# Kernel tuning notes

Hardware: AMD Instinct MI355X
Metric: run time of the kernel (lower is better)

## Reference

```python
import jax, jax.numpy as jnp
import numpy as np
from jax import lax

EPS = 1e-6

def build_hh_matrix(V):
    """V: [d, d] rows are (unnormalized) Householder vectors.
    Returns Q = prod_i (I - 2 v_i v_i^T) applied left-to-right, matching
    the torch loop Q <- Q @ (I - 2 v v^T) == Q - 2 (Q v) v^T (rank-1 update)."""
    d = V.shape[0]
    Vn = V / (jnp.linalg.norm(V, axis=1, keepdims=True) + EPS)
    def step(Q, v):
        Qv = Q @ v                      # [d]
        return Q - 2.0 * jnp.outer(Qv, v), None
    Q, _ = lax.scan(step, jnp.eye(d, dtype=V.dtype), Vn)
    return Q


def setup_inputs() -> dict:
    key = jax.random.key(0)
    k1, k2 = jax.random.split(key)
    x = jax.random.normal(k1, (131072, 512), dtype=jnp.float32)
    hd_vecs = jax.random.normal(k2, (1, 512, 512), dtype=jnp.float32)
    return {"x": x, "hd_vecs": hd_vecs}


def reference(x, hd_vecs):
    # n_mat == 1 branch: out = (Q @ x^T)^T = x @ Q^T
    Q = build_hh_matrix(hd_vecs[0])     # [d, d]
    return x @ Q.T                      # [npatches, d]
```

## Files before the change

kernel.cpp:

```cpp
#include <hip/hip_runtime.h>
#include <hip/hip_bf16.h>
#include <stdint.h>

#define EPS 1e-6f

typedef unsigned short ushort_t;
using frag  = __attribute__((ext_vector_type(8))) short;
using f32x4 = __attribute__((ext_vector_type(4))) float;
using fv4   = __attribute__((ext_vector_type(4))) float;

__device__ __forceinline__ ushort_t f2bf(float f) {
  uint32_t u = __builtin_bit_cast(uint32_t, f);
  u += 0x7FFFu + ((u >> 16) & 1u);
  return (ushort_t)(u >> 16);
}

__global__ __launch_bounds__(256) void normalize_kernel(const float* __restrict__ V,
                                                        float* __restrict__ Vn) {
  const int gw   = blockIdx.x * 4 + (threadIdx.x >> 6);
  const int lane = threadIdx.x & 63;
  const float4* src = (const float4*)(V + gw * 512) + lane * 2;
  float4 a = src[0], c = src[1];
  float s = a.x*a.x + a.y*a.y + a.z*a.z + a.w*a.w
          + c.x*c.x + c.y*c.y + c.z*c.z + c.w*c.w;
  #pragma unroll
  for (int off = 32; off; off >>= 1) s += __shfl_xor(s, off);
  float inv = 1.f / (sqrtf(s) + EPS);
  float4 na = make_float4(a.x*inv, a.y*inv, a.z*inv, a.w*inv);
  float4 nc = make_float4(c.x*inv, c.y*inv, c.z*inv, c.w*inv);
  float4* dst = (float4*)(Vn + gw * 512) + lane * 2;
  dst[0] = na; dst[1] = nc;
}

__global__ __launch_bounds__(256) void gram_kernel(const float* __restrict__ Vn,
                                                   float* __restrict__ G) {
  const int gw   = blockIdx.x * 4 + (threadIdx.x >> 6);
  const int b    = gw >> 7, i = gw & 127;
  const int lane = threadIdx.x & 63;
  const float4* ri = (const float4*)(Vn + (b * 128 + i) * 512) + lane * 2;
  float4 a0 = ri[0], a1 = ri[1];
  #pragma unroll 2
  for (int j = i + 1; j < 128; ++j) {
    const float4* rj = (const float4*)(Vn + (b * 128 + j) * 512) + lane * 2;
    float4 c0 = rj[0], c1 = rj[1];
    float s = a0.x*c0.x + a0.y*c0.y + a0.z*c0.z + a0.w*c0.w
            + a1.x*c1.x + a1.y*c1.y + a1.z*c1.z + a1.w*c1.w;
    #pragma unroll
    for (int off = 32; off; off >>= 1) s += __shfl_xor(s, off);
    if (lane == 0) G[(b * 128 + i) * 128 + j] = s;
  }
}

__global__ __launch_bounds__(256) void trinv_kernel(float* __restrict__ GT) {
  __shared__ float Gs[128][132];
  __shared__ float Ai[64][68];
  __shared__ float Di[64][68];
  __shared__ float C1[64][68];
  const int b = blockIdx.x, tid = threadIdx.x;
  float* Gg = GT + b * 16384;

  {
    const int r = tid >> 1, h = tid & 1;
    const float4* src = (const float4*)(Gg + r * 128 + h * 64);
    float4* dst = (float4*)(&Gs[r][h * 64]);
    #pragma unroll
    for (int e = 0; e < 16; ++e) dst[e] = src[e];
  }
  __syncthreads();

  const int wave = tid >> 6, lane = tid & 63;
  if (wave < 2) {
    const int o = wave * 64;
    float t[64];
    #pragma unroll
    for (int i = 63; i >= 0; --i) {
      float s = (i == lane) ? 1.f : 0.f;
      #pragma unroll
      for (int j = i + 1; j < 64; ++j) s -= Gs[o + i][o + j] * t[j];
      t[i] = 2.f * s;
    }
    float (*OUT)[68] = wave ? Di : Ai;
    #pragma unroll
    for (int i = 0; i < 64; ++i) OUT[i][lane] = t[i];
  }
  __syncthreads();

  const int i0 = (tid >> 4) << 2;
  const int j0 = (tid & 15) << 2;

  {
    fv4 acc[4] = {};
    for (int l = 0; l < 64; l += 4) {
      fv4 g[4], d[4];
      #pragma unroll
      for (int r = 0; r < 4; ++r) g[r] = *(const fv4*)(&Gs[i0 + r][64 + l]);
      #pragma unroll
      for (int r = 0; r < 4; ++r) d[r] = *(const fv4*)(&Di[l + r][j0]);
      #pragma unroll
      for (int r = 0; r < 4; ++r)
        #pragma unroll
        for (int l2 = 0; l2 < 4; ++l2)
          #pragma unroll
          for (int q = 0; q < 4; ++q)
            acc[r][q] = fmaf(g[r][l2], d[l2][q], acc[r][q]);
    }
    #pragma unroll
    for (int r = 0; r < 4; ++r) *(fv4*)(&C1[i0 + r][j0]) = acc[r];
  }
  __syncthreads();

  {
    fv4 acc[4] = {};
    for (int l = 0; l < 64; l += 4) {
      fv4 g[4], d[4];
      #pragma unroll
      for (int r = 0; r < 4; ++r) g[r] = *(const fv4*)(&Ai[i0 + r][l]);
      #pragma unroll
      for (int r = 0; r < 4; ++r) d[r] = *(const fv4*)(&C1[l + r][j0]);
      #pragma unroll
      for (int r = 0; r < 4; ++r)
        #pragma unroll
        for (int l2 = 0; l2 < 4; ++l2)
          #pragma unroll
          for (int q = 0; q < 4; ++q)
            acc[r][q] = fmaf(g[r][l2], d[l2][q], acc[r][q]);
    }
    #pragma unroll
    for (int r = 0; r < 4; ++r)
      #pragma unroll
      for (int q = 0; q < 4; ++q)
        Gg[(64 + j0 + q) * 128 + (i0 + r)] = -acc[r][q];
  }

  {
    const int j = tid >> 1, h = tid & 1;
    if (j < 64) {
      if (h == 0) { for (int i = 0; i < 64; ++i) Gg[j * 128 + i] = Ai[i][j]; }
      else        { for (int i = 0; i < 64; ++i) Gg[j * 128 + 64 + i] = 0.f; }
    } else if (h == 1) {
      for (int i = 0; i < 64; ++i) Gg[j * 128 + 64 + i] = Di[i][j - 64];
    }
  }
}

__global__ __launch_bounds__(256) void chain_kernel(const float* __restrict__ Vn,
                                                    const float* __restrict__ Tt,
                                                    ushort_t* __restrict__ Qf) {
  __shared__ float Qt[4][512];
  __shared__ float Vc[32768];
  __shared__ float Pp[4][4][64];
  __shared__ float Ps[4][128];
  __shared__ float Asm[4][128];
  const int t = threadIdx.x, w = t >> 6, lane = t & 63;
  const int m0 = blockIdx.x * 4;
  char* VcB = (char*)Vc;

  for (int idx = t; idx < 2048; idx += 256) {
    int i = idx >> 9, k = idx & 511;
    Qt[i][k] = (m0 + i == k) ? 1.f : 0.f;
  }

  for (int b = 0; b < 4; ++b) {
    if (b == 0) {
      __syncthreads();
      if (t < 128) {
        #pragma unroll
        for (int i = 0; i < 4; ++i) Ps[i][t] = Vn[t * 512 + m0 + i];
      }
      __syncthreads();
    } else {
      for (int ch = 0; ch < 2; ++ch) {
        __syncthreads();
        #pragma unroll 4
        for (int q = 0; q < 32; ++q) {
          int s = q * 256 + t;
          int r = s >> 7, c4 = s & 127;
          float4 v = *(const float4*)(Vn + (b * 128 + ch * 64 + r) * 512 + c4 * 4);
          *(float4*)(VcB + r * 2048 + ((c4 * 16) ^ ((r & 7) << 4))) = v;
        }
        __syncthreads();
        float pa[4] = {0.f, 0.f, 0.f, 0.f};
        #pragma unroll 4
        for (int k4 = 0; k4 < 32; ++k4) {
          int kk = w * 128 + k4 * 4;
          float4 vv = *(const float4*)(VcB + lane * 2048 + ((kk * 4) ^ ((lane & 7) << 4)));
          #pragma unroll
          for (int i = 0; i < 4; ++i) {
            float4 qq = *(const float4*)(&Qt[i][kk]);
            pa[i] += qq.x*vv.x + qq.y*vv.y + qq.z*vv.z + qq.w*vv.w;
          }
        }
        #pragma unroll
        for (int i = 0; i < 4; ++i) Pp[w][i][lane] = pa[i];
        __syncthreads();
        if (w < 2) {
          #pragma unroll
          for (int i2 = 0; i2 < 2; ++i2) {
            int i = w * 2 + i2;
            Ps[i][ch * 64 + lane] = Pp[0][i][lane] + Pp[1][i][lane]
                                  + Pp[2][i][lane] + Pp[3][i][lane];
          }
        }
      }
      __syncthreads();
    }
    {
      const float* trow = Tt + b * 16384 + (t >> 1) * 128 + (t & 1) * 64;
      float aa[4] = {0.f, 0.f, 0.f, 0.f};
      #pragma unroll 4
      for (int j4 = 0; j4 < 16; ++j4) {
        float4 tv = *(const float4*)(trow + j4 * 4);
        int j = (t & 1) * 64 + j4 * 4;
        #pragma unroll
        for (int i = 0; i < 4; ++i) {
          float4 pv = *(const float4*)(&Ps[i][j]);
          aa[i] += pv.x*tv.x + pv.y*tv.y + pv.z*tv.z + pv.w*tv.w;
        }
      }
      #pragma unroll
      for (int i = 0; i < 4; ++i) {
        float o = __shfl_xor(aa[i], 1);
        if ((t & 1) == 0) Asm[i][t >> 1] = aa[i] + o;
      }
    }
    for (int ch = 0; ch < 2; ++ch) {
      __syncthreads();
      #pragma unroll 4
      for (int q = 0; q < 32; ++q) {
        int s = q * 256 + t;
        int r = s >> 7, c4 = s & 127;
        float4 v = *(const float4*)(Vn + (b * 128 + ch * 64 + r) * 512 + c4 * 4);
        *(float4*)(VcB + r * 2048 + ((c4 * 16) ^ ((r & 7) << 4))) = v;
      }
      __syncthreads();
      float acc0[4] = {0.f,0.f,0.f,0.f}, acc1[4] = {0.f,0.f,0.f,0.f};
      #pragma unroll 4
      for (int n = 0; n < 64; ++n) {
        float2 vv = *(const float2*)(VcB + n * 2048 + ((t * 8) ^ ((n & 7) << 4)));
        #pragma unroll
        for (int i = 0; i < 4; ++i) {
          float a = Asm[i][ch * 64 + n];
          acc0[i] = fmaf(a, vv.x, acc0[i]);
          acc1[i] = fmaf(a, vv.y, acc1[i]);
        }
      }
      #pragma unroll
      for (int i = 0; i < 4; ++i) {
        Qt[i][t * 2]     -= acc0[i];
        Qt[i][t * 2 + 1] -= acc1[i];
      }
    }
  }
  __syncthreads();
  {
    int i = t >> 6, ks = (t >> 2) & 15, lg = t & 3;
    int r = m0 + i;
    int nt = r >> 4, l = lg * 16 + (r & 15);
    const float* src = &Qt[i][ks * 32 + lg * 8];
    frag v;
    #pragma unroll
    for (int j = 0; j < 8; ++j) v[j] = (short)f2bf(src[j]);
    *(frag*)(Qf + ((size_t)(ks * 32 + nt) * 64 + l) * 8) = v;
  }
}

__global__ __launch_bounds__(512, 4) void final_gemm(const float* __restrict__ X,
                                                     const ushort_t* __restrict__ Qf,
                                                     float* __restrict__ out) {
  __shared__ __align__(16) ushort_t As[2][64 * 64];
  const int tid = threadIdx.x;
  const int w = tid >> 6, lane = tid & 63;
  const int m0 = blockIdx.x * 64;
  const int row = tid >> 3, seg = tid & 7;

  f32x4 acc[4][4];
  #pragma unroll
  for (int i = 0; i < 4; ++i)
    #pragma unroll
    for (int j = 0; j < 4; ++j) acc[i][j] = (f32x4){0.f, 0.f, 0.f, 0.f};

  {
    const float4* src = (const float4*)(X + (m0 + row) * 512 + seg * 8);
    float4 f0 = src[0], f1 = src[1];
    frag v;
    v[0]=(short)f2bf(f0.x); v[1]=(short)f2bf(f0.y); v[2]=(short)f2bf(f0.z); v[3]=(short)f2bf(f0.w);
    v[4]=(short)f2bf(f1.x); v[5]=(short)f2bf(f1.y); v[6]=(short)f2bf(f1.z); v[7]=(short)f2bf(f1.w);
    *(frag*)((char*)As[0] + row * 128 + ((seg * 16) ^ ((row & 7) << 4))) = v;
  }

  int cur = 0;
  for (int kt = 0; kt < 8; ++kt) {
    float4 f0, f1;
    if (kt < 7) {
      const float4* src = (const float4*)(X + (m0 + row) * 512 + (kt + 1) * 64 + seg * 8);
      f0 = src[0]; f1 = src[1];
    }
    __syncthreads();

    #pragma unroll
    for (int ks2 = 0; ks2 < 2; ++ks2) {
      const int ks = kt * 2 + ks2;
      frag bfr[4];
      #pragma unroll
      for (int j = 0; j < 4; ++j) {
        int nt = w * 4 + j;
        bfr[j] = *(const frag*)(Qf + ((size_t)(ks * 32 + nt) * 64 + lane) * 8);
      }
      frag a[4];
      const int kb = ks2 * 64 + ((lane >> 4) << 4);
      #pragma unroll
      for (int mf = 0; mf < 4; ++mf) {
        int r = mf * 16 + (lane & 15);
        a[mf] = *(const frag*)((const char*)As[cur] + r * 128 + (kb ^ ((r & 7) << 4)));
      }
      #pragma unroll
      for (int mf = 0; mf < 4; ++mf)
        #pragma unroll
        for (int j = 0; j < 4; ++j)
          acc[mf][j] = __builtin_amdgcn_mfma_f32_16x16x32_bf16(a[mf], bfr[j], acc[mf][j], 0, 0, 0);
    }

    if (kt < 7) {
      frag v;
      v[0]=(short)f2bf(f0.x); v[1]=(short)f2bf(f0.y); v[2]=(short)f2bf(f0.z); v[3]=(short)f2bf(f0.w);
      v[4]=(short)f2bf(f1.x); v[5]=(short)f2bf(f1.y); v[6]=(short)f2bf(f1.z); v[7]=(short)f2bf(f1.w);
      *(frag*)((char*)As[cur ^ 1] + row * 128 + ((seg * 16) ^ ((row & 7) << 4))) = v;
      cur ^= 1;
    }
  }

  #pragma unroll
  for (int mf = 0; mf < 4; ++mf) {
    int rbase = m0 + mf * 16 + ((lane >> 4) << 2);
    #pragma unroll
    for (int j = 0; j < 4; ++j) {
      int col = w * 64 + j * 16 + (lane & 15);
      #pragma unroll
      for (int r = 0; r < 4; ++r)
        out[(size_t)(rbase + r) * 512 + col] = acc[mf][j][r];
    }
  }
}

extern "C" void kernel_launch(void* const* d_in, const int* in_sizes, int n_in,
                              void* d_out, int out_size, void* d_ws, size_t ws_size,
                              hipStream_t stream) {
  const float* x = (const float*)d_in[0];
  const float* V = (const float*)d_in[1];
  float* out = (float*)d_out;
  float* ws  = (float*)d_ws;

  float*    Vn = ws;
  float*    GT = ws + 262144;
  ushort_t* Qf = (ushort_t*)(ws + 327680);

  normalize_kernel<<<128, 256, 0, stream>>>(V, Vn);
  gram_kernel<<<128, 256, 0, stream>>>(Vn, GT);
  trinv_kernel<<<4, 256, 0, stream>>>(GT);
  chain_kernel<<<128, 256, 0, stream>>>(Vn, GT, Qf);
  final_gemm<<<2048, 512, 0, stream>>>(x, Qf, out);
}
```

Baseline: 337.8 us.

## Stage GEMM epilogue through LDS, prefetch two tiles, parallelize gram, drop chain LDS staging

The final GEMM now routes each 16-row slab of output through an LDS buffer so global stores become full-row float4 writes. It prefetches X two k-tiles ahead into registers, unrolls the k loop, and swaps __syncthreads for a raw barrier plus lgkmcnt wait. The gram kernel uses one block per row with four waves striding over j, launching 512 blocks. The chain kernel reads Vn straight from global (L2) instead of copying 128 KB into shared memory. The extra LDS lowers the final GEMM occupancy target from 4 to 3 blocks per CU, and removing chain staging trades fewer syncs for more global reads.

Measured after the change: 294.5 us. -12.8%, faster.

```diff
diff --git a/kernel.cpp b/kernel.cpp
--- a/kernel.cpp
+++ b/kernel.cpp
@@ -9,17 +9,26 @@
 using f32x4 = __attribute__((ext_vector_type(4))) float;
 using fv4   = __attribute__((ext_vector_type(4))) float;
 
+#define SWAITLG() asm volatile("s_waitcnt lgkmcnt(0)" ::: "memory")
+
 __device__ __forceinline__ ushort_t f2bf(float f) {
   uint32_t u = __builtin_bit_cast(uint32_t, f);
   u += 0x7FFFu + ((u >> 16) & 1u);
   return (ushort_t)(u >> 16);
 }
 
+__device__ __forceinline__ frag pack8(float4 f0, float4 f1) {
+  frag v;
+  v[0]=(short)f2bf(f0.x); v[1]=(short)f2bf(f0.y); v[2]=(short)f2bf(f0.z); v[3]=(short)f2bf(f0.w);
+  v[4]=(short)f2bf(f1.x); v[5]=(short)f2bf(f1.y); v[6]=(short)f2bf(f1.z); v[7]=(short)f2bf(f1.w);
+  return v;
+}
+
 __global__ __launch_bounds__(256) void normalize_kernel(const float* __restrict__ V,
                                                         float* __restrict__ Vn) {
   const int gw   = blockIdx.x * 4 + (threadIdx.x >> 6);
   const int lane = threadIdx.x & 63;
-  const float4* src = (const float4*)(V + gw * 512) + lane * 2;
+  const float4* src = (const float4*)(V + (size_t)gw * 512) + lane * 2;
   float4 a = src[0], c = src[1];
   float s = a.x*a.x + a.y*a.y + a.z*a.z + a.w*a.w
           + c.x*c.x + c.y*c.y + c.z*c.z + c.w*c.w;
@@ -28,26 +37,25 @@
   float inv = 1.f / (sqrtf(s) + EPS);
   float4 na = make_float4(a.x*inv, a.y*inv, a.z*inv, a.w*inv);
   float4 nc = make_float4(c.x*inv, c.y*inv, c.z*inv, c.w*inv);
-  float4* dst = (float4*)(Vn + gw * 512) + lane * 2;
+  float4* dst = (float4*)(Vn + (size_t)gw * 512) + lane * 2;
   dst[0] = na; dst[1] = nc;
 }
 
 __global__ __launch_bounds__(256) void gram_kernel(const float* __restrict__ Vn,
                                                    float* __restrict__ G) {
-  const int gw   = blockIdx.x * 4 + (threadIdx.x >> 6);
-  const int b    = gw >> 7, i = gw & 127;
-  const int lane = threadIdx.x & 63;
-  const float4* ri = (const float4*)(Vn + (b * 128 + i) * 512) + lane * 2;
+  const int gi = blockIdx.x;
+  const int b = gi >> 7, i = gi & 127;
+  const int w = threadIdx.x >> 6, lane = threadIdx.x & 63;
+  const float4* ri = (const float4*)(Vn + (size_t)gi * 512) + lane * 2;
   float4 a0 = ri[0], a1 = ri[1];
-  #pragma unroll 2
-  for (int j = i + 1; j < 128; ++j) {
-    const float4* rj = (const float4*)(Vn + (b * 128 + j) * 512) + lane * 2;
+  for (int j = i + 1 + w; j < 128; j += 4) {
+    const float4* rj = (const float4*)(Vn + (size_t)(b * 128 + j) * 512) + lane * 2;
     float4 c0 = rj[0], c1 = rj[1];
     float s = a0.x*c0.x + a0.y*c0.y + a0.z*c0.z + a0.w*c0.w
             + a1.x*c1.x + a1.y*c1.y + a1.z*c1.z + a1.w*c1.w;
     #pragma unroll
     for (int off = 32; off; off >>= 1) s += __shfl_xor(s, off);
-    if (lane == 0) G[(b * 128 + i) * 128 + j] = s;
+    if (lane == 0) G[(size_t)gi * 128 + j] = s;
   }
 }
 
@@ -147,13 +155,11 @@
                                                     const float* __restrict__ Tt,
                                                     ushort_t* __restrict__ Qf) {
   __shared__ float Qt[4][512];
-  __shared__ float Vc[32768];
   __shared__ float Pp[4][4][64];
   __shared__ float Ps[4][128];
   __shared__ float Asm[4][128];
   const int t = threadIdx.x, w = t >> 6, lane = t & 63;
   const int m0 = blockIdx.x * 4;
-  char* VcB = (char*)Vc;
 
   for (int idx = t; idx < 2048; idx += 256) {
     int i = idx >> 9, k = idx & 511;
@@ -171,19 +177,13 @@
     } else {
       for (int ch = 0; ch < 2; ++ch) {
         __syncthreads();
-        #pragma unroll 4
-        for (int q = 0; q < 32; ++q) {
-          int s = q * 256 + t;
-          int r = s >> 7, c4 = s & 127;
-          float4 v = *(const float4*)(Vn + (b * 128 + ch * 64 + r) * 512 + c4 * 4);
-          *(float4*)(VcB + r * 2048 + ((c4 * 16) ^ ((r & 7) << 4))) = v;
-        }
-        __syncthreads();
+        const int n = ch * 64 + lane;
+        const float* vrow = Vn + (size_t)(b * 128 + n) * 512;
         float pa[4] = {0.f, 0.f, 0.f, 0.f};
-        #pragma unroll 4
+        #pragma unroll 8
         for (int k4 = 0; k4 < 32; ++k4) {
           int kk = w * 128 + k4 * 4;
-          float4 vv = *(const float4*)(VcB + lane * 2048 + ((kk * 4) ^ ((lane & 7) << 4)));
+          float4 vv = *(const float4*)(vrow + kk);
           #pragma unroll
           for (int i = 0; i < 4; ++i) {
             float4 qq = *(const float4*)(&Qt[i][kk]);
@@ -223,23 +223,16 @@
         if ((t & 1) == 0) Asm[i][t >> 1] = aa[i] + o;
       }
     }
-    for (int ch = 0; ch < 2; ++ch) {
-      __syncthreads();
+    __syncthreads();
+    {
+      float acc0[4] = {0.f,0.f,0.f,0.f}, acc1[4] = {0.f,0.f,0.f,0.f};
+      const float* vb = Vn + (size_t)b * 65536 + t * 2;
       #pragma unroll 4
-      for (int q = 0; q < 32; ++q) {
-        int s = q * 256 + t;
-        int r = s >> 7, c4 = s & 127;
-        float4 v = *(const float4*)(Vn + (b * 128 + ch * 64 + r) * 512 + c4 * 4);
-        *(float4*)(VcB + r * 2048 + ((c4 * 16) ^ ((r & 7) << 4))) = v;
-      }
-      __syncthreads();
-      float acc0[4] = {0.f,0.f,0.f,0.f}, acc1[4] = {0.f,0.f,0.f,0.f};
-      #pragma unroll 4
-      for (int n = 0; n < 64; ++n) {
-        float2 vv = *(const float2*)(VcB + n * 2048 + ((t * 8) ^ ((n & 7) << 4)));
+      for (int n = 0; n < 128; ++n) {
+        float2 vv = *(const float2*)(vb + (size_t)n * 512);
         #pragma unroll
         for (int i = 0; i < 4; ++i) {
-          float a = Asm[i][ch * 64 + n];
+          float a = Asm[i][n];
           acc0[i] = fmaf(a, vv.x, acc0[i]);
           acc1[i] = fmaf(a, vv.y, acc1[i]);
         }
@@ -264,14 +257,17 @@
   }
 }
 
-__global__ __launch_bounds__(512, 4) void final_gemm(const float* __restrict__ X,
+__global__ __launch_bounds__(512, 3) void final_gemm(const float* __restrict__ X,
                                                      const ushort_t* __restrict__ Qf,
                                                      float* __restrict__ out) {
   __shared__ __align__(16) ushort_t As[2][64 * 64];
+  __shared__ __align__(16) float Ep[16][516];
   const int tid = threadIdx.x;
   const int w = tid >> 6, lane = tid & 63;
   const int m0 = blockIdx.x * 64;
   const int row = tid >> 3, seg = tid & 7;
+  const int sw_off = row * 128 + ((seg * 16) ^ ((row & 7) << 4));
+  const float4* xs = (const float4*)(X + (size_t)(m0 + row) * 512) + seg * 2;
 
   f32x4 acc[4][4];
   #pragma unroll
@@ -279,35 +275,29 @@
     #pragma unroll
     for (int j = 0; j < 4; ++j) acc[i][j] = (f32x4){0.f, 0.f, 0.f, 0.f};
 
-  {
-    const float4* src = (const float4*)(X + (m0 + row) * 512 + seg * 8);
-    float4 f0 = src[0], f1 = src[1];
-    frag v;
-    v[0]=(short)f2bf(f0.x); v[1]=(short)f2bf(f0.y); v[2]=(short)f2bf(f0.z); v[3]=(short)f2bf(f0.w);
-    v[4]=(short)f2bf(f1.x); v[5]=(short)f2bf(f1.y); v[6]=(short)f2bf(f1.z); v[7]=(short)f2bf(f1.w);
-    *(frag*)((char*)As[0] + row * 128 + ((seg * 16) ^ ((row & 7) << 4))) = v;
-  }
-
-  int cur = 0;
+  float4 fE0 = xs[0], fE1 = xs[1];
+  float4 fO0 = xs[16], fO1 = xs[17];
+  *(frag*)((char*)As[0] + sw_off) = pack8(fE0, fE1);
+  SWAITLG();
+  __builtin_amdgcn_s_barrier();
+
+  #pragma unroll
   for (int kt = 0; kt < 8; ++kt) {
-    float4 f0, f1;
-    if (kt < 7) {
-      const float4* src = (const float4*)(X + (m0 + row) * 512 + (kt + 1) * 64 + seg * 8);
-      f0 = src[0]; f1 = src[1];
-    }
-    __syncthreads();
-
-    #pragma unroll
-    for (int ks2 = 0; ks2 < 2; ++ks2) {
-      const int ks = kt * 2 + ks2;
-      frag bfr[4];
-      #pragma unroll
-      for (int j = 0; j < 4; ++j) {
-        int nt = w * 4 + j;
-        bfr[j] = *(const frag*)(Qf + ((size_t)(ks * 32 + nt) * 64 + lane) * 8);
-      }
-      frag a[4];
-      const int kb = ks2 * 64 + ((lane >> 4) << 4);
+    const int cur = kt & 1;
+    frag b0[4], b1[4];
+    #pragma unroll
+    for (int j = 0; j < 4; ++j) {
+      int nt = w * 4 + j;
+      b0[j] = *(const frag*)(Qf + ((size_t)((2*kt)     * 32 + nt) * 64 + lane) * 8);
+      b1[j] = *(const frag*)(Qf + ((size_t)((2*kt + 1) * 32 + nt) * 64 + lane) * 8);
+    }
+    if (kt < 6) {
+      if (cur == 0) { fE0 = xs[(kt + 2) * 16]; fE1 = xs[(kt + 2) * 16 + 1]; }
+      else          { fO0 = xs[(kt + 2) * 16]; fO1 = xs[(kt + 2) * 16 + 1]; }
+    }
+    frag a[4];
+    {
+      const int kb = (lane >> 4) << 4;
       #pragma unroll
       for (int mf = 0; mf < 4; ++mf) {
         int r = mf * 16 + (lane & 15);
@@ -317,27 +307,48 @@
       for (int mf = 0; mf < 4; ++mf)
         #pragma unroll
         for (int j = 0; j < 4; ++j)
-          acc[mf][j] = __builtin_amdgcn_mfma_f32_16x16x32_bf16(a[mf], bfr[j], acc[mf][j], 0, 0, 0);
-    }
-
+          acc[mf][j] = __builtin_amdgcn_mfma_f32_16x16x32_bf16(a[mf], b0[j], acc[mf][j], 0, 0, 0);
+    }
+    {
+      const int kb = 64 + ((lane >> 4) << 4);
+      #pragma unroll
+      for (int mf = 0; mf < 4; ++mf) {
+        int r = mf * 16 + (lane & 15);
+        a[mf] = *(const frag*)((const char*)As[cur] + r * 128 + (kb ^ ((r & 7) << 4)));
+      }
+      #pragma unroll
+      for (int mf = 0; mf < 4; ++mf)
+        #pragma unroll
+        for (int j = 0; j < 4; ++j)
+          acc[mf][j] = __builtin_amdgcn_mfma_f32_16x16x32_bf16(a[mf], b1[j], acc[mf][j], 0, 0, 0);
+    }
     if (kt < 7) {
-      frag v;
-      v[0]=(short)f2bf(f0.x); v[1]=(short)f2bf(f0.y); v[2]=(short)f2bf(f0.z); v[3]=(short)f2bf(f0.w);
-      v[4]=(short)f2bf(f1.x); v[5]=(short)f2bf(f1.y); v[6]=(short)f2bf(f1.z); v[7]=(short)f2bf(f1.w);
-      *(frag*)((char*)As[cur ^ 1] + row * 128 + ((seg * 16) ^ ((row & 7) << 4))) = v;
-      cur ^= 1;
-    }
+      float4 c0 = (cur == 0) ? fO0 : fE0;
+      float4 c1 = (cur == 0) ? fO1 : fE1;
+      *(frag*)((char*)As[cur ^ 1] + sw_off) = pack8(c0, c1);
+    }
+    SWAITLG();
+    __builtin_amdgcn_s_barrier();
   }
 
   #pragma unroll
   for (int mf = 0; mf < 4; ++mf) {
-    int rbase = m0 + mf * 16 + ((lane >> 4) << 2);
+    if (mf > 0) __builtin_amdgcn_s_barrier();
     #pragma unroll
     for (int j = 0; j < 4; ++j) {
       int col = w * 64 + j * 16 + (lane & 15);
       #pragma unroll
       for (int r = 0; r < 4; ++r)
-        out[(size_t)(rbase + r) * 512 + col] = acc[mf][j][r];
+        Ep[((lane >> 4) << 2) + r][col] = acc[mf][j][r];
+    }
+    SWAITLG();
+    __builtin_amdgcn_s_barrier();
+    #pragma unroll
+    for (int e = 0; e < 4; ++e) {
+      int idx = e * 512 + tid;
+      int rr = idx >> 7, c4 = idx & 127;
+      float4 v = *(const float4*)(&Ep[rr][c4 * 4]);
+      *(float4*)(out + (size_t)(m0 + mf * 16 + rr) * 512 + c4 * 4) = v;
     }
   }
 }
@@ -355,7 +366,7 @@
   ushort_t* Qf = (ushort_t*)(ws + 327680);
 
   normalize_kernel<<<128, 256, 0, stream>>>(V, Vn);
-  gram_kernel<<<128, 256, 0, stream>>>(Vn, GT);
+  gram_kernel<<<512, 256, 0, stream>>>(Vn, GT);
   trinv_kernel<<<4, 256, 0, stream>>>(GT);
   chain_kernel<<<128, 256, 0, stream>>>(Vn, GT, Qf);
   final_gemm<<<2048, 512, 0, stream>>>(x, Qf, out);
```
